# Kernel tuning notes

Hardware: AMD Instinct MI355X
Metric: run time of the kernel (lower is better)

## Reference

```python
import jax, jax.numpy as jnp
import numpy as np

D = 1024
H = 16
DH = D // H
L = 128  # max_pos_len
B = 4
T = 1024
SCALE = float(np.sqrt(D / H))


def setup_inputs() -> dict:
    key = jax.random.key(0)
    ks = jax.random.split(key, 9)
    x_q = jax.random.normal(ks[0], (B, T, D), dtype=jnp.float32)
    x_k = jax.random.normal(ks[1], (B, T, D), dtype=jnp.float32)
    x_v = jax.random.normal(ks[2], (B, T, D), dtype=jnp.float32)
    mask = jax.random.randint(ks[3], (B, 1, 1, T), 0, 2) == 1  # bool, True = masked
    Wq = jax.random.normal(ks[4], (D, D), dtype=jnp.float32) * 0.02
    Wk = jax.random.normal(ks[5], (D, D), dtype=jnp.float32) * 0.02
    Wv = jax.random.normal(ks[6], (D, D), dtype=jnp.float32) * 0.02
    Wo = jax.random.normal(ks[7], (D, D), dtype=jnp.float32) * 0.02
    pos_emb = jax.random.normal(ks[8], (2 * L + 1, DH), dtype=jnp.float32)
    return {"x_q": x_q, "x_k": x_k, "x_v": x_v, "mask": mask,
            "Wq": Wq, "Wk": Wk, "Wv": Wv, "Wo": Wo, "pos_emb": pos_emb}


def reference(x_q, x_k, x_v, mask, Wq, Wk, Wv, Wo, pos_emb):
    # nn.Linear(bias=False): y = x @ W.T
    def split_heads(x):  # (B,T,D) -> (B,H,T,DH)
        return x.reshape(B, -1, H, DH).transpose(0, 2, 1, 3)

    Q = split_heads(x_q @ Wq.T)
    K = split_heads(x_k @ Wk.T)
    V = split_heads(x_v @ Wv.T)

    logits = jnp.einsum('bhqd,bhkd->bhqk', Q, K)

    # arrange_char_pos_embedding: indices[q,k] = clamp(k-q, -L, L) + L
    rel = jnp.clip(jnp.arange(T)[None, :] - jnp.arange(T)[:, None], -L, L) + L
    arranged_pos = pos_emb[rel]  # (T_Q, T_K, DH)
    pos_logits = jnp.einsum('bhqd,qkd->bhqk', Q, arranged_pos)

    logits = (logits + pos_logits) / SCALE
    logits = jnp.where(mask, -jnp.inf, logits)  # mask broadcasts (B,1,1,T)
    attn = jax.nn.softmax(logits, axis=-1)  # dropout p=0.0 -> identity

    combined = jnp.einsum('bhqk,bhkd->bhqd', attn, V)
    heads_concat = combined.transpose(0, 2, 1, 3).reshape(B, -1, D)
    return heads_concat @ Wo.T
```

## Files before the change

### kernel.cpp

```cpp
#include <hip/hip_runtime.h>
#include <hip/hip_bf16.h>
#include <stdint.h>

typedef __attribute__((ext_vector_type(8))) short short8;
typedef __attribute__((ext_vector_type(4))) float f32x4;

__device__ __forceinline__ uint16_t f2bf(float f) {
    union { float f; uint32_t u; } v; v.f = f;
    uint32_t r = v.u + 0x7FFF + ((v.u >> 16) & 1);
    return (uint16_t)(r >> 16);
}
__device__ __forceinline__ float bf2f(uint16_t u) {
    union { uint32_t u; float f; } v; v.u = ((uint32_t)u) << 16;
    return v.f;
}

template<int F32>
__device__ __forceinline__ uint4 load8(const void* p, size_t off) {
    if (F32) {
        const float* f = (const float*)p + off;
        float4 f0 = *(const float4*)f;
        float4 f1 = *(const float4*)(f + 4);
        uint4 r;
        r.x = (uint32_t)f2bf(f0.x) | ((uint32_t)f2bf(f0.y) << 16);
        r.y = (uint32_t)f2bf(f0.z) | ((uint32_t)f2bf(f0.w) << 16);
        r.z = (uint32_t)f2bf(f1.x) | ((uint32_t)f2bf(f1.y) << 16);
        r.w = (uint32_t)f2bf(f1.z) | ((uint32_t)f2bf(f1.w) << 16);
        return r;
    } else {
        return *(const uint4*)((const uint16_t*)p + off);
    }
}

#define GLDS(gp, lp) __builtin_amdgcn_global_load_lds( \
    (const __attribute__((address_space(1))) void*)(gp), \
    (__attribute__((address_space(3))) void*)(lp), 16, 0, 0)

struct CvtSeg { const float* s; uint16_t* d; int n8; };
struct CvtArgs { CvtSeg seg[9]; int nseg; const void* mraw; int* mcanon; };

__global__ __launch_bounds__(256) void cvt_bf16(CvtArgs a)
{
    if (blockIdx.x == 0) {
        __shared__ int flags[3];
        const uint32_t* w = (const uint32_t*)a.mraw;
        const uint8_t* b8 = (const uint8_t*)a.mraw;
        const int t = threadIdx.x;
        if (t < 3) flags[t] = 0;
        __syncthreads();
        int fbyte = 0, ff32 = 0, fodd = 0;
        for (int i = t; i < 1024; i += 256) {
            uint32_t v = w[i];
            if (v != 0u && v != 1u && v != 0x3F800000u) fbyte = 1;
            if (v == 0x3F800000u) ff32 = 1;
            if ((i & 1) && v != 0u) fodd = 1;
        }
        if (fbyte) atomicOr(&flags[0], 1);
        if (ff32)  atomicOr(&flags[1], 1);
        if (fodd)  atomicOr(&flags[2], 1);
        __syncthreads();
        int mode;
        if (flags[0]) mode = 1;
        else if (flags[1]) mode = 0;
        else if (!flags[2]) mode = 2;
        else mode = 0;
        for (int k = t; k < 4096; k += 256) {
            int val;
            if (mode == 1)      val = (b8[k] != 0);
            else if (mode == 2) val = (w[2 * k] != 0u);
            else                val = (w[k] != 0u);
            a.mcanon[k] = val;
        }
    }
    const int tid = blockIdx.x * 256 + threadIdx.x;
    const int stride = gridDim.x * 256;
    for (int s = 0; s < a.nseg; ++s) {
        const float* src = a.seg[s].s;
        uint16_t* dst = a.seg[s].d;
        const int n8 = a.seg[s].n8;
        if (src) {
            for (int i = tid; i < n8; i += stride)
                *(uint4*)(dst + (size_t)i * 8) = load8<1>(src, (size_t)i * 8);
        } else {
            const uint4 z = {0u, 0u, 0u, 0u};
            for (int i = tid; i < n8; i += stride)
                *(uint4*)(dst + (size_t)i * 8) = z;
        }
    }
}

__device__ __forceinline__ void gemm128_body(
    const uint16_t* __restrict__ A, const uint16_t* __restrict__ B,
    void* __restrict__ C, int M, int N, int K, int cm, int bm, int bn,
    uint16_t* As, uint16_t* Bs)
{
    const int t = threadIdx.x;
    const int lane = t & 63, wave = t >> 6;
    const int lrow = lane & 15, quad = lane >> 4;
    const int wr = (wave >> 1) * 64, wc = (wave & 1) * 64;

    const int g_row = wave * 16 + (lane >> 2);
    const int g_col = (lane & 3) * 8;

    const f32x4 fz = {0.f, 0.f, 0.f, 0.f};
    f32x4 acc[4][4];
#pragma unroll
    for (int i = 0; i < 4; ++i)
#pragma unroll
        for (int j = 0; j < 4; ++j) acc[i][j] = fz;

    for (int k0 = 0; k0 < K; k0 += 32) {
        __syncthreads();
        GLDS(A + (size_t)(bm * 128 + g_row) * K + k0 + g_col,      As + wave * 512);
        GLDS(A + (size_t)(bm * 128 + g_row + 64) * K + k0 + g_col, As + wave * 512 + 2048);
        GLDS(B + (size_t)(bn * 128 + g_row) * K + k0 + g_col,      Bs + wave * 512);
        GLDS(B + (size_t)(bn * 128 + g_row + 64) * K + k0 + g_col, Bs + wave * 512 + 2048);
        __syncthreads();

        short8 a[4], b[4];
#pragma unroll
        for (int i = 0; i < 4; ++i)
            a[i] = *(const short8*)(As + (wr + i * 16 + lrow) * 32 + quad * 8);
#pragma unroll
        for (int j = 0; j < 4; ++j)
            b[j] = *(const short8*)(Bs + (wc + j * 16 + lrow) * 32 + quad * 8);
#pragma unroll
        for (int i = 0; i < 4; ++i)
#pragma unroll
            for (int j = 0; j < 4; ++j)
                acc[i][j] = __builtin_amdgcn_mfma_f32_16x16x32_bf16(a[i], b[j], acc[i][j], 0, 0, 0);
    }

    if (cm == 2) {
        __syncthreads();
        uint16_t* scr = As + wave * 1024;
#pragma unroll
        for (int i = 0; i < 4; ++i)
#pragma unroll
            for (int j = 0; j < 4; ++j) {
                uint2 pk;
                pk.x = (uint32_t)f2bf(acc[i][j][0]) | ((uint32_t)f2bf(acc[i][j][1]) << 16);
                pk.y = (uint32_t)f2bf(acc[i][j][2]) | ((uint32_t)f2bf(acc[i][j][3]) << 16);
                *(uint2*)(scr + lrow * 16 + quad * 4) = pk;
                if (lane < 32) {
                    int n = lane >> 1, m8 = (lane & 1) * 8;
                    short8 vv = *(const short8*)(scr + n * 16 + m8);
                    int ng = bn * 128 + wc + j * 16 + n;
                    int hh = ng >> 6, d = ng & 63;
                    int mg = bm * 128 + wr + i * 16;
                    int bb = mg >> 10, tl = (mg & 1023) + m8;
                    *(short8*)((uint16_t*)C +
                        ((((size_t)bb * 16 + hh) * 64 + d) * 1024 + tl)) = vv;
                }
            }
        return;
    }

#pragma unroll
    for (int i = 0; i < 4; ++i)
#pragma unroll
        for (int j = 0; j < 4; ++j)
#pragma unroll
            for (int r = 0; r < 4; ++r) {
                int m = bm * 128 + wr + i * 16 + quad * 4 + r;
                int n = bn * 128 + wc + j * 16 + lrow;
                float val = acc[i][j][r];
                if (cm == 0) {
                    ((float*)C)[(size_t)m * N + n] = val;
                } else {
                    int bb = m >> 10, tt = m & 1023, hh = n >> 6, d = n & 63;
                    ((uint16_t*)C)[(((size_t)bb * 16 + hh) * 1024 + tt) * 64 + d] = f2bf(val);
                }
            }
}

__global__ __launch_bounds__(256) void gemm128_qkv(
    const uint16_t* __restrict__ xq, const uint16_t* __restrict__ xk, const uint16_t* __restrict__ xv,
    const uint16_t* __restrict__ Wq, const uint16_t* __restrict__ Wk, const uint16_t* __restrict__ Wv,
    uint16_t* __restrict__ Qh, uint16_t* __restrict__ Khd, uint16_t* __restrict__ Vt)
{
    __shared__ alignas(16) uint16_t As[128 * 32];
    __shared__ alignas(16) uint16_t Bs[128 * 32];
    const int z = blockIdx.z;
    const uint16_t* A = (z == 0) ? xq : (z == 1) ? xk : xv;
    const uint16_t* B = (z == 0) ? Wq : (z == 1) ? Wk : Wv;
    void* C = (z == 0) ? (void*)Qh : (z == 1) ? (void*)Khd : (void*)Vt;
    const int cm = (z == 2) ? 2 : 1;
    gemm128_body(A, B, C, 4096, 1024, 1024, cm, blockIdx.x, blockIdx.y, As, Bs);
}

__global__ __launch_bounds__(256) void gemm128_single(
    const uint16_t* __restrict__ A, const uint16_t* __restrict__ B, void* __restrict__ C,
    int M, int N, int K)
{
    __shared__ alignas(16) uint16_t As[128 * 32];
    __shared__ alignas(16) uint16_t Bs[128 * 32];
    gemm128_body(A, B, C, M, N, K, 0, blockIdx.x, blockIdx.y, As, Bs);
}

__global__ __launch_bounds__(256) void flash_attn(
    const uint16_t* __restrict__ Qh, const uint16_t* __restrict__ Kh,
    const uint16_t* __restrict__ Vt, const uint16_t* __restrict__ pos,
    const int* __restrict__ mask, uint16_t* __restrict__ comb)
{
    const int blk = blockIdx.x;
    const int bh = blk >> 4;
    const int qt = blk & 15;
    const int b = bh >> 4;
    const int h = bh & 15;
    const int t = threadIdx.x;
    const int lane = t & 63;
    const int wave = t >> 6;
    const int lrow = lane & 15;
    const int quad = lane >> 4;
    const int qb = qt * 64 + wave * 16;

    __shared__ alignas(16) uint16_t Ks[2 * 64 * 32];
    __shared__ alignas(16) uint16_t Vs[2 * 64 * 32];
    __shared__ alignas(16) uint16_t Qpos_l[64][274];
    __shared__ alignas(16) uint16_t Pl[4][16][72];

    const uint16_t* Qp = Qh + ((size_t)bh * 1024 + qb) * 64;
    short8 aq0 = *(const short8*)(Qp + (size_t)lrow * 64 + quad * 8);
    short8 aq1 = *(const short8*)(Qp + (size_t)lrow * 64 + 32 + quad * 8);

    const f32x4 fz = {0.f, 0.f, 0.f, 0.f};

#pragma unroll 4
    for (int nt = 0; nt < 17; ++nt) {
        short8 pb0 = *(const short8*)(pos + (size_t)(nt * 16 + lrow) * 64 + quad * 8);
        short8 pb1 = *(const short8*)(pos + (size_t)(nt * 16 + lrow) * 64 + 32 + quad * 8);
        f32x4 c = __builtin_amdgcn_mfma_f32_16x16x32_bf16(aq0, pb0, fz, 0, 0, 0);
        c = __builtin_amdgcn_mfma_f32_16x16x32_bf16(aq1, pb1, c, 0, 0, 0);
#pragma unroll
        for (int r = 0; r < 4; ++r)
            Qpos_l[wave * 16 + quad * 4 + r][nt * 16 + lrow] = f2bf(c[r]);
    }

    float pcl[4], pch[4];
#pragma unroll
    for (int r = 0; r < 4; ++r) {
        int ql = wave * 16 + quad * 4 + r;
        pcl[r] = bf2f(Qpos_l[ql][0])   * 0.125f;
        pch[r] = bf2f(Qpos_l[ql][256]) * 0.125f;
    }

    const uint16_t* Kp = Kh + (size_t)bh * 65536;
    const uint16_t* Vp = Vt + (size_t)bh * 65536;
    const int* mk = mask + b * 1024;

    const int sg_r = lane >> 2;
    const int sg_c = (lane & 3) * 8;
    const int hw = wave >> 1;
    const int gw = (wave & 1) * 2;

    f32x4 o[4] = {fz, fz, fz, fz};
    float lsum[4] = {0.f, 0.f, 0.f, 0.f};

    for (int kb = 0; kb < 1024; kb += 64) {
        __syncthreads();
#pragma unroll
        for (int gg = 0; gg < 2; ++gg) {
            int g = gw + gg;
            GLDS(Kp + (size_t)(kb + g * 16 + sg_r) * 64 + hw * 32 + sg_c,
                 Ks + hw * 2048 + g * 512);
            GLDS(Vp + (size_t)(g * 16 + sg_r) * 1024 + kb + hw * 32 + sg_c,
                 Vs + hw * 2048 + g * 512);
        }
        __syncthreads();

        f32x4 s[4];
#pragma unroll
        for (int j = 0; j < 4; ++j) {
            short8 k0 = *(const short8*)(Ks + (j * 16 + lrow) * 32 + quad * 8);
            short8 k1 = *(const short8*)(Ks + 2048 + (j * 16 + lrow) * 32 + quad * 8);
            s[j] = __builtin_amdgcn_mfma_f32_16x16x32_bf16(aq0, k0, fz, 0, 0, 0);
            s[j] = __builtin_amdgcn_mfma_f32_16x16x32_bf16(aq1, k1, s[j], 0, 0, 0);
        }

        const int diff = kb - qb;
        if (diff <= -192 || diff >= 144) {
            const bool low = (diff <= -192);
#pragma unroll
            for (int j = 0; j < 4; ++j) {
                const int key = kb + j * 16 + lrow;
                const bool m = (mk[key] != 0);
#pragma unroll
                for (int r = 0; r < 4; ++r) {
                    float pc = low ? pcl[r] : pch[r];
                    float e = m ? 0.f : __expf(__builtin_fmaf(s[j][r], 0.125f, pc));
                    lsum[r] += e;
                    Pl[wave][quad * 4 + r][j * 16 + lrow] = f2bf(e);
                }
            }
        } else {
#pragma unroll
            for (int j = 0; j < 4; ++j) {
                const int key = kb + j * 16 + lrow;
                const bool m = (mk[key] != 0);
#pragma unroll
                for (int r = 0; r < 4; ++r) {
                    int q = qb + quad * 4 + r;
                    int ql = q & 63;
                    int rel = min(max(key - q, -128), 128) + 128;
                    float p = bf2f(Qpos_l[ql][rel]);
                    float e = m ? 0.f : __expf((s[j][r] + p) * 0.125f);
                    lsum[r] += e;
                    Pl[wave][quad * 4 + r][j * 16 + lrow] = f2bf(e);
                }
            }
        }
        short8 ap0 = *(const short8*)(&Pl[wave][lrow][quad * 8]);
        short8 ap1 = *(const short8*)(&Pl[wave][lrow][32 + quad * 8]);

#pragma unroll
        for (int dt = 0; dt < 4; ++dt) {
            short8 v0 = *(const short8*)(Vs + (dt * 16 + lrow) * 32 + quad * 8);
            short8 v1 = *(const short8*)(Vs + 2048 + (dt * 16 + lrow) * 32 + quad * 8);
            o[dt] = __builtin_amdgcn_mfma_f32_16x16x32_bf16(ap0, v0, o[dt], 0, 0, 0);
            o[dt] = __builtin_amdgcn_mfma_f32_16x16x32_bf16(ap1, v1, o[dt], 0, 0, 0);
        }
    }

#pragma unroll
    for (int off = 1; off < 16; off <<= 1)
#pragma unroll
        for (int r = 0; r < 4; ++r)
            lsum[r] += __shfl_xor(lsum[r], off);

    float inv[4];
#pragma unroll
    for (int r = 0; r < 4; ++r) inv[r] = 1.0f / lsum[r];

#pragma unroll
    for (int dt = 0; dt < 4; ++dt)
#pragma unroll
        for (int r = 0; r < 4; ++r) {
            size_t row = (size_t)b * 1024 + qb + quad * 4 + r;
            size_t col = (size_t)h * 64 + dt * 16 + lrow;
            comb[row * 1024 + col] = f2bf(o[dt][r] * inv[r]);
        }
}

extern "C" void kernel_launch(void* const* d_in, const int* in_sizes, int n_in,
                              void* d_out, int out_size, void* d_ws, size_t ws_size,
                              hipStream_t stream)
{
    const float* x_q = (const float*)d_in[0];
    const float* x_k = (const float*)d_in[1];
    const float* x_v = (const float*)d_in[2];
    const void*  msk = d_in[3];
    const float* Wq  = (const float*)d_in[4];
    const float* Wk  = (const float*)d_in[5];
    const float* Wv  = (const float*)d_in[6];
    const float* Wo  = (const float*)d_in[7];
    const float* pos = (const float*)d_in[8];

    char* ws = (char*)d_ws;
    const size_t MB = 1u << 20;
    uint16_t* Qh   = (uint16_t*)(ws);
    uint16_t* Khd  = (uint16_t*)(ws + 8 * MB);
    uint16_t* Vt   = (uint16_t*)(ws + 16 * MB);
    uint16_t* xqb  = (uint16_t*)(ws + 24 * MB);
    uint16_t* xkb  = (uint16_t*)(ws + 32 * MB);
    uint16_t* xvb  = (uint16_t*)(ws + 40 * MB);
    uint16_t* Wqb  = (uint16_t*)(ws + 48 * MB);
    uint16_t* Wkb  = (uint16_t*)(ws + 50 * MB);
    uint16_t* Wvb  = (uint16_t*)(ws + 52 * MB);
    uint16_t* Wob  = (uint16_t*)(ws + 54 * MB);
    uint16_t* posb = (uint16_t*)(ws + 56 * MB);
    int*      canon = (int*)(ws + 56 * MB + 65536);
    uint16_t* comb = xqb;

    CvtArgs ca{};
    int ns = 0;
    ca.seg[ns++] = {x_q, xqb, 524288};
    ca.seg[ns++] = {x_k, xkb, 524288};
    ca.seg[ns++] = {x_v, xvb, 524288};
    ca.seg[ns++] = {Wq, Wqb, 131072};
    ca.seg[ns++] = {Wk, Wkb, 131072};
    ca.seg[ns++] = {Wv, Wvb, 131072};
    ca.seg[ns++] = {Wo, Wob, 131072};
    ca.seg[ns++] = {pos, posb, 2056};
    ca.seg[ns++] = {nullptr, posb + 16448, 120};
    ca.nseg = ns;
    ca.mraw = msk;
    ca.mcanon = canon;
    cvt_bf16<<<dim3(512), dim3(256), 0, stream>>>(ca);

    gemm128_qkv<<<dim3(32, 8, 3), dim3(256), 0, stream>>>(
        xqb, xkb, xvb, Wqb, Wkb, Wvb, Qh, Khd, Vt);

    flash_attn<<<dim3(1024), dim3(256), 0, stream>>>(Qh, Khd, Vt, posb, canon, comb);

    gemm128_single<<<dim3(32, 8), dim3(256), 0, stream>>>(
        comb, Wob, d_out, 4096, 1024, 1024);
}
```

Before: 255.7 us.

## Double-buffer K/V tiles in attention and use 64x128 tiles for output GEMM

The attention kernel now keeps two LDS buffers for K and V. It prefetches the next 64-key tile while computing on the current one, which cuts the per-iteration barriers from two to one and hides global-to-LDS latency behind the MFMA and softmax work. The output projection gets its own kernel with 64x128 block tiles, so it launches twice as many blocks and fills the CUs better on the 4096x1024 GEMM. The shared gemm body is inlined into the QKV kernel. The cost is more LDS in the attention kernel, which may lower occupancy, and less reuse per block in the output GEMM.

```diff
diff --git a/kernel.cpp b/kernel.cpp
--- a/kernel.cpp
+++ b/kernel.cpp
@@ -89,16 +89,26 @@
     }
 }
 
-__device__ __forceinline__ void gemm128_body(
-    const uint16_t* __restrict__ A, const uint16_t* __restrict__ B,
-    void* __restrict__ C, int M, int N, int K, int cm, int bm, int bn,
-    uint16_t* As, uint16_t* Bs)
+__global__ __launch_bounds__(256) void gemm128_qkv(
+    const uint16_t* __restrict__ xq, const uint16_t* __restrict__ xk, const uint16_t* __restrict__ xv,
+    const uint16_t* __restrict__ Wq, const uint16_t* __restrict__ Wk, const uint16_t* __restrict__ Wv,
+    uint16_t* __restrict__ Qh, uint16_t* __restrict__ Khd, uint16_t* __restrict__ Vt)
 {
+    __shared__ alignas(16) uint16_t As[128 * 32];
+    __shared__ alignas(16) uint16_t Bs[128 * 32];
+
+    const int z = blockIdx.z;
+    const uint16_t* A = (z == 0) ? xq : (z == 1) ? xk : xv;
+    const uint16_t* B = (z == 0) ? Wq : (z == 1) ? Wk : Wv;
+    uint16_t* C = (z == 0) ? Qh : (z == 1) ? Khd : Vt;
+    const int cm = (z == 2) ? 2 : 1;
+    const int bm = blockIdx.x, bn = blockIdx.y;
+    const int K = 1024;
+
     const int t = threadIdx.x;
     const int lane = t & 63, wave = t >> 6;
     const int lrow = lane & 15, quad = lane >> 4;
     const int wr = (wave >> 1) * 64, wc = (wave & 1) * 64;
-
     const int g_row = wave * 16 + (lane >> 2);
     const int g_col = (lane & 3) * 8;
 
@@ -149,8 +159,7 @@
                     int hh = ng >> 6, d = ng & 63;
                     int mg = bm * 128 + wr + i * 16;
                     int bb = mg >> 10, tl = (mg & 1023) + m8;
-                    *(short8*)((uint16_t*)C +
-                        ((((size_t)bb * 16 + hh) * 64 + d) * 1024 + tl)) = vv;
+                    *(short8*)(C + ((((size_t)bb * 16 + hh) * 64 + d) * 1024 + tl)) = vv;
                 }
             }
         return;
@@ -164,38 +173,64 @@
             for (int r = 0; r < 4; ++r) {
                 int m = bm * 128 + wr + i * 16 + quad * 4 + r;
                 int n = bn * 128 + wc + j * 16 + lrow;
-                float val = acc[i][j][r];
-                if (cm == 0) {
-                    ((float*)C)[(size_t)m * N + n] = val;
-                } else {
-                    int bb = m >> 10, tt = m & 1023, hh = n >> 6, d = n & 63;
-                    ((uint16_t*)C)[(((size_t)bb * 16 + hh) * 1024 + tt) * 64 + d] = f2bf(val);
-                }
-            }
-}
-
-__global__ __launch_bounds__(256) void gemm128_qkv(
-    const uint16_t* __restrict__ xq, const uint16_t* __restrict__ xk, const uint16_t* __restrict__ xv,
-    const uint16_t* __restrict__ Wq, const uint16_t* __restrict__ Wk, const uint16_t* __restrict__ Wv,
-    uint16_t* __restrict__ Qh, uint16_t* __restrict__ Khd, uint16_t* __restrict__ Vt)
+                int bb = m >> 10, tt = m & 1023, hh = n >> 6, d = n & 63;
+                C[(((size_t)bb * 16 + hh) * 1024 + tt) * 64 + d] = f2bf(acc[i][j][r]);
+            }
+}
+
+__global__ __launch_bounds__(256) void gemm_out(
+    const uint16_t* __restrict__ A, const uint16_t* __restrict__ B,
+    float* __restrict__ C, int M, int N, int K)
 {
-    __shared__ alignas(16) uint16_t As[128 * 32];
+    __shared__ alignas(16) uint16_t As[64 * 32];
     __shared__ alignas(16) uint16_t Bs[128 * 32];
-    const int z = blockIdx.z;
-    const uint16_t* A = (z == 0) ? xq : (z == 1) ? xk : xv;
-    const uint16_t* B = (z == 0) ? Wq : (z == 1) ? Wk : Wv;
-    void* C = (z == 0) ? (void*)Qh : (z == 1) ? (void*)Khd : (void*)Vt;
-    const int cm = (z == 2) ? 2 : 1;
-    gemm128_body(A, B, C, 4096, 1024, 1024, cm, blockIdx.x, blockIdx.y, As, Bs);
-}
-
-__global__ __launch_bounds__(256) void gemm128_single(
-    const uint16_t* __restrict__ A, const uint16_t* __restrict__ B, void* __restrict__ C,
-    int M, int N, int K)
-{
-    __shared__ alignas(16) uint16_t As[128 * 32];
-    __shared__ alignas(16) uint16_t Bs[128 * 32];
-    gemm128_body(A, B, C, M, N, K, 0, blockIdx.x, blockIdx.y, As, Bs);
+
+    const int t = threadIdx.x;
+    const int lane = t & 63, wave = t >> 6;
+    const int lrow = lane & 15, quad = lane >> 4;
+    const int wr = (wave >> 1) * 32, wc = (wave & 1) * 64;
+    const int g_row = wave * 16 + (lane >> 2);
+    const int g_col = (lane & 3) * 8;
+    const int bm = blockIdx.x, bn = blockIdx.y;
+
+    const f32x4 fz = {0.f, 0.f, 0.f, 0.f};
+    f32x4 acc[2][4];
+#pragma unroll
+    for (int i = 0; i < 2; ++i)
+#pragma unroll
+        for (int j = 0; j < 4; ++j) acc[i][j] = fz;
+
+    for (int k0 = 0; k0 < K; k0 += 32) {
+        __syncthreads();
+        GLDS(A + (size_t)(bm * 64 + g_row) * K + k0 + g_col,       As + wave * 512);
+        GLDS(B + (size_t)(bn * 128 + g_row) * K + k0 + g_col,      Bs + wave * 512);
+        GLDS(B + (size_t)(bn * 128 + g_row + 64) * K + k0 + g_col, Bs + wave * 512 + 2048);
+        __syncthreads();
+
+        short8 a[2], b[4];
+#pragma unroll
+        for (int i = 0; i < 2; ++i)
+            a[i] = *(const short8*)(As + (wr + i * 16 + lrow) * 32 + quad * 8);
+#pragma unroll
+        for (int j = 0; j < 4; ++j)
+            b[j] = *(const short8*)(Bs + (wc + j * 16 + lrow) * 32 + quad * 8);
+#pragma unroll
+        for (int i = 0; i < 2; ++i)
+#pragma unroll
+            for (int j = 0; j < 4; ++j)
+                acc[i][j] = __builtin_amdgcn_mfma_f32_16x16x32_bf16(a[i], b[j], acc[i][j], 0, 0, 0);
+    }
+
+#pragma unroll
+    for (int i = 0; i < 2; ++i)
+#pragma unroll
+        for (int j = 0; j < 4; ++j)
+#pragma unroll
+            for (int r = 0; r < 4; ++r) {
+                int m = bm * 64 + wr + i * 16 + quad * 4 + r;
+                int n = bn * 128 + wc + j * 16 + lrow;
+                C[(size_t)m * N + n] = acc[i][j][r];
+            }
 }
 
 __global__ __launch_bounds__(256) void flash_attn(
@@ -215,10 +250,26 @@
     const int quad = lane >> 4;
     const int qb = qt * 64 + wave * 16;
 
-    __shared__ alignas(16) uint16_t Ks[2 * 64 * 32];
-    __shared__ alignas(16) uint16_t Vs[2 * 64 * 32];
+    __shared__ alignas(16) uint16_t Ks[2][4096];
+    __shared__ alignas(16) uint16_t Vs[2][4096];
     __shared__ alignas(16) uint16_t Qpos_l[64][274];
     __shared__ alignas(16) uint16_t Pl[4][16][72];
+
+    const uint16_t* Kp = Kh + (size_t)bh * 65536;
+    const uint16_t* Vp = Vt + (size_t)bh * 65536;
+    const int* mk = mask + b * 1024;
+
+    const int sg_r = lane >> 2;
+    const int sg_c = (lane & 3) * 8;
+    const int hw = wave >> 1;
+    const int gw = (wave & 1) * 2;
+
+#pragma unroll
+    for (int gg = 0; gg < 2; ++gg) {
+        int g = gw + gg;
+        GLDS(Kp + (size_t)(g * 16 + sg_r) * 64 + hw * 32 + sg_c, &Ks[0][hw * 2048 + g * 512]);
+        GLDS(Vp + (size_t)(g * 16 + sg_r) * 1024 + hw * 32 + sg_c, &Vs[0][hw * 2048 + g * 512]);
+    }
 
     const uint16_t* Qp = Qh + ((size_t)bh * 1024 + qb) * 64;
     short8 aq0 = *(const short8*)(Qp + (size_t)lrow * 64 + quad * 8);
@@ -245,35 +296,31 @@
         pch[r] = bf2f(Qpos_l[ql][256]) * 0.125f;
     }
 
-    const uint16_t* Kp = Kh + (size_t)bh * 65536;
-    const uint16_t* Vp = Vt + (size_t)bh * 65536;
-    const int* mk = mask + b * 1024;
-
-    const int sg_r = lane >> 2;
-    const int sg_c = (lane & 3) * 8;
-    const int hw = wave >> 1;
-    const int gw = (wave & 1) * 2;
-
     f32x4 o[4] = {fz, fz, fz, fz};
     float lsum[4] = {0.f, 0.f, 0.f, 0.f};
 
     for (int kb = 0; kb < 1024; kb += 64) {
-        __syncthreads();
-#pragma unroll
-        for (int gg = 0; gg < 2; ++gg) {
-            int g = gw + gg;
-            GLDS(Kp + (size_t)(kb + g * 16 + sg_r) * 64 + hw * 32 + sg_c,
-                 Ks + hw * 2048 + g * 512);
-            GLDS(Vp + (size_t)(g * 16 + sg_r) * 1024 + kb + hw * 32 + sg_c,
-                 Vs + hw * 2048 + g * 512);
-        }
-        __syncthreads();
+        const int cur = (kb >> 6) & 1;
+        __syncthreads();
+        if (kb + 64 < 1024) {
+            const int nxt = cur ^ 1;
+#pragma unroll
+            for (int gg = 0; gg < 2; ++gg) {
+                int g = gw + gg;
+                GLDS(Kp + (size_t)(kb + 64 + g * 16 + sg_r) * 64 + hw * 32 + sg_c,
+                     &Ks[nxt][hw * 2048 + g * 512]);
+                GLDS(Vp + (size_t)(g * 16 + sg_r) * 1024 + kb + 64 + hw * 32 + sg_c,
+                     &Vs[nxt][hw * 2048 + g * 512]);
+            }
+        }
+        const uint16_t* Kc = Ks[cur];
+        const uint16_t* Vc = Vs[cur];
 
         f32x4 s[4];
 #pragma unroll
         for (int j = 0; j < 4; ++j) {
-            short8 k0 = *(const short8*)(Ks + (j * 16 + lrow) * 32 + quad * 8);
-            short8 k1 = *(const short8*)(Ks + 2048 + (j * 16 + lrow) * 32 + quad * 8);
+            short8 k0 = *(const short8*)(Kc + (j * 16 + lrow) * 32 + quad * 8);
+            short8 k1 = *(const short8*)(Kc + 2048 + (j * 16 + lrow) * 32 + quad * 8);
             s[j] = __builtin_amdgcn_mfma_f32_16x16x32_bf16(aq0, k0, fz, 0, 0, 0);
             s[j] = __builtin_amdgcn_mfma_f32_16x16x32_bf16(aq1, k1, s[j], 0, 0, 0);
         }
@@ -315,8 +362,8 @@
 
 #pragma unroll
         for (int dt = 0; dt < 4; ++dt) {
-            short8 v0 = *(const short8*)(Vs + (dt * 16 + lrow) * 32 + quad * 8);
-            short8 v1 = *(const short8*)(Vs + 2048 + (dt * 16 + lrow) * 32 + quad * 8);
+            short8 v0 = *(const short8*)(Vc + (dt * 16 + lrow) * 32 + quad * 8);
+            short8 v1 = *(const short8*)(Vc + 2048 + (dt * 16 + lrow) * 32 + quad * 8);
             o[dt] = __builtin_amdgcn_mfma_f32_16x16x32_bf16(ap0, v0, o[dt], 0, 0, 0);
             o[dt] = __builtin_amdgcn_mfma_f32_16x16x32_bf16(ap1, v1, o[dt], 0, 0, 0);
         }
@@ -393,6 +440,6 @@
 
     flash_attn<<<dim3(1024), dim3(256), 0, stream>>>(Qh, Khd, Vt, posb, canon, comb);
 
-    gemm128_single<<<dim3(32, 8), dim3(256), 0, stream>>>(
-        comb, Wob, d_out, 4096, 1024, 1024);
-}
+    gemm_out<<<dim3(64, 8), dim3(256), 0, stream>>>(
+        comb, Wob, (float*)d_out, 4096, 1024, 1024);
+}
```

Measured after the change: 254.6 us. About the same (-0.4%).
